# Optimization experiments

Hardware: AMD Instinct MI355X
Metric: run time of the kernel (lower is better)

## Reference

```python
import jax, jax.numpy as jnp
import numpy as np

B, S, D, H, E, K = 4, 2048, 1024, 4096, 4, 2


def setup_inputs() -> dict:
    key = jax.random.key(0)
    ks = jax.random.split(key, 7)
    s1 = 1.0 / np.sqrt(D)  # torch Linear default init bound for fan_in=D
    s2 = 1.0 / np.sqrt(H)
    return {
        "x": jax.random.normal(ks[0], (B, S, D), jnp.float32),
        "w1": jax.random.uniform(ks[1], (E, D, H), jnp.float32, -s1, s1),
        "b1": jax.random.uniform(ks[2], (E, H), jnp.float32, -s1, s1),
        "w2": jax.random.uniform(ks[3], (E, H, D), jnp.float32, -s2, s2),
        "b2": jax.random.uniform(ks[4], (E, D), jnp.float32, -s2, s2),
        "wr": jax.random.uniform(ks[5], (D, E), jnp.float32, -s1, s1),
        "br": jax.random.uniform(ks[6], (E,), jnp.float32, -s1, s1),
    }


def reference(x, w1, b1, w2, b2, wr, br):
    # Faithful to the naive torch SparseMoE (noisy_gating=False):
    #   out += gates[:, i, None] * expert_j(x_flat * mask_ij)  for all i, j
    # Key observation: expert_j applied to a zeroed row gives the constant
    #   c_j = W2_j @ gelu(b1_j) + b2_j  (torch GELU is the exact erf form),
    # so for token t routed (at slot i) to expert e = idx[t, i]:
    #   sum_j expert_j(x_t * mask) = FFN_e(x_t) - c_e + sum_j c_j
    # This reproduces the original math exactly while running each expert's
    # dense FFN over ALL tokens (the naive compute pattern).
    Bx, Sx, Dx = x.shape
    xf = x.reshape(-1, Dx)                                   # [N, D]
    logits = xf @ wr + br                                    # [N, E]
    topk_vals, topk_idx = jax.lax.top_k(logits, K)           # [N, K]
    gates = jax.nn.softmax(topk_vals, axis=-1)               # [N, K]

    # Dense per-expert FFN over all tokens (naive MoE compute)
    h = jax.nn.gelu(jnp.einsum('nd,edh->enh', xf, w1) + b1[:, None, :],
                    approximate=False)                       # [E, N, H]
    y = jnp.einsum('enh,ehd->end', h, w2) + b2[:, None, :]   # [E, N, D]

    # expert_j(0) constants
    c = jnp.einsum('eh,ehd->ed', jax.nn.gelu(b1, approximate=False), w2) + b2  # [E, D]
    c_sum = c.sum(axis=0)                                    # [D]

    yt = jnp.transpose(y, (1, 0, 2))                         # [N, E, D]
    y_sel = jnp.take_along_axis(yt, topk_idx[:, :, None], axis=1)  # [N, K, D]
    c_sel = c[topk_idx]                                      # [N, K, D]

    out = jnp.einsum('nk,nkd->nd', gates, y_sel - c_sel + c_sum[None, None, :])
    return out.reshape(Bx, Sx, Dx)
```

## Files before the change

### kernel.cpp

```cpp
#include <hip/hip_runtime.h>

#define N_TOK 8192
#define DIM   1024
#define HID   4096
#define NEXP  4
#define MAXT  68
#define NSLOT (MAXT*256)

typedef __attribute__((ext_vector_type(8))) _Float16 f16x8;
typedef __attribute__((ext_vector_type(4))) _Float16 f16x4;
typedef __attribute__((ext_vector_type(4))) float    f32x4;

__device__ __forceinline__ float gelu_erf(float v){
    return 0.5f * v * (1.0f + erff(v * 0.70710678118654752440f));
}
__device__ __forceinline__ float gelu_tanh(float v){
    float u = 0.7978845608028654f * v * (1.0f + 0.044715f * v * v);
    float e = __expf(2.0f * u);
    float t = 1.0f - 2.0f / (e + 1.0f);
    return 0.5f * v * (1.0f + t);
}

#define GLDS16(g, s) __builtin_amdgcn_global_load_lds( \
    (const __attribute__((address_space(1))) void*)(g), \
    (__attribute__((address_space(3))) void*)(s), 16, 0, 0)

#define BARRIER() do{ __builtin_amdgcn_s_barrier(); asm volatile("" ::: "memory"); }while(0)
#define VMCNTN(n) asm volatile("s_waitcnt vmcnt(" #n ")" ::: "memory")

__global__ void k_transpose_all(const float* __restrict__ w1, const float* __restrict__ w2,
                                _Float16* __restrict__ w1t, _Float16* __restrict__ w2t){
    __shared__ float tile[32][33];
    int bid = blockIdx.x;
    int z = bid >> 12;
    int i = bid & 4095;
    const float* s; _Float16* d; int R, C, bx, by;
    if (z < 4){ R = DIM; C = HID; bx = i & 127; by = i >> 7;
        s = w1 + (size_t)z * R * C; d = w1t + (size_t)z * R * C; }
    else      { R = HID; C = DIM; bx = i & 31;  by = i >> 5;
        s = w2 + (size_t)(z-4) * R * C; d = w2t + (size_t)(z-4) * R * C; }
    int tx = threadIdx.x & 31, ty = threadIdx.x >> 5;
    int c0 = bx*32, r0 = by*32;
    #pragma unroll
    for (int rr = 0; rr < 32; rr += 8)
        tile[ty+rr][tx] = s[(size_t)(r0+ty+rr)*C + c0+tx];
    __syncthreads();
    #pragma unroll
    for (int rr = 0; rr < 32; rr += 8)
        d[(size_t)(c0+ty+rr)*R + r0+tx] = (_Float16)tile[tx][ty+rr];
}

__global__ void k_gb1(const float* __restrict__ b1, float* __restrict__ gb1, int n){
    int i = blockIdx.x*256 + threadIdx.x;
    if (i < n) gb1[i] = gelu_erf(b1[i]);
}

__global__ void k_cprime_part(const float* __restrict__ w2, const float* __restrict__ gb1,
                              float* __restrict__ part){
    int d = blockIdx.x*256 + threadIdx.x;
    int p = blockIdx.y, e = blockIdx.z;
    float acc = 0.f;
    int h0 = p*(HID/8);
    for (int h = h0; h < h0 + HID/8; ++h)
        acc += gb1[e*HID + h] * w2[((size_t)e*HID + h)*DIM + d];
    part[(size_t)(e*8 + p)*DIM + d] = acc;
}

__global__ void k_cfinal(const float* __restrict__ part, const float* __restrict__ b2,
                         float* __restrict__ cprime, float* __restrict__ csum){
    int d = blockIdx.x*256 + threadIdx.x;
    float cs = 0.f;
    #pragma unroll
    for (int e = 0; e < NEXP; ++e){
        float a = 0.f;
        #pragma unroll
        for (int p = 0; p < 8; ++p) a += part[(size_t)(e*8 + p)*DIM + d];
        cprime[e*DIM + d] = a;
        cs += a + b2[e*DIM + d];
    }
    csum[d] = cs;
}

__global__ void k_route(const float* __restrict__ x, const float* __restrict__ wr,
                        const float* __restrict__ br, _Float16* __restrict__ xb,
                        int* __restrict__ expi, float* __restrict__ gatev){
    int lane = threadIdx.x & 63, w = threadIdx.x >> 6;
    int t = blockIdx.x*4 + w;
    const float4* x4  = (const float4*)(x + (size_t)t*DIM);
    const float4* wr4 = (const float4*)wr;
    f16x4* xb4 = (f16x4*)(xb + (size_t)t*DIM);
    float a0=0.f, a1=0.f, a2=0.f, a3=0.f;
    #pragma unroll
    for (int it = 0; it < 4; ++it){
        int q = it*64 + lane;
        float4 v = x4[q];
        f16x4 h; h[0]=(_Float16)v.x; h[1]=(_Float16)v.y; h[2]=(_Float16)v.z; h[3]=(_Float16)v.w;
        xb4[q] = h;
        int d = q*4;
        float4 w0 = wr4[d], w1v = wr4[d+1], w2v = wr4[d+2], w3v = wr4[d+3];
        a0 += v.x*w0.x + v.y*w1v.x + v.z*w2v.x + v.w*w3v.x;
        a1 += v.x*w0.y + v.y*w1v.y + v.z*w2v.y + v.w*w3v.y;
        a2 += v.x*w0.z + v.y*w1v.z + v.z*w2v.z + v.w*w3v.z;
        a3 += v.x*w0.w + v.y*w1v.w + v.z*w2v.w + v.w*w3v.w;
    }
    #pragma unroll
    for (int off = 32; off; off >>= 1){
        a0 += __shfl_xor(a0, off);
        a1 += __shfl_xor(a1, off);
        a2 += __shfl_xor(a2, off);
        a3 += __shfl_xor(a3, off);
    }
    if (lane == 0){
        float v[4] = {a0+br[0], a1+br[1], a2+br[2], a3+br[3]};
        int e0 = 0; float v0 = v[0];
        #pragma unroll
        for (int e = 1; e < 4; ++e) if (v[e] > v0){ v0 = v[e]; e0 = e; }
        int e1 = -1; float v1 = -1e30f;
        #pragma unroll
        for (int e = 0; e < 4; ++e) if (e != e0 && v[e] > v1){ v1 = v[e]; e1 = e; }
        float ex = expf(v1 - v0);
        float g0 = 1.f/(1.f+ex), g1 = ex/(1.f+ex);
        expi[2*t] = e0; expi[2*t+1] = e1;
        gatev[2*t] = g0; gatev[2*t+1] = g1;
    }
}

__global__ __launch_bounds__(1024)
void k_compact(const int* __restrict__ expi, const float* __restrict__ gatev,
               int* __restrict__ tbase, int* __restrict__ tokl, int* __restrict__ slotof){
    const int e = blockIdx.x;
    const int tid = threadIdx.x, lane = tid & 63, wv = tid >> 6;
    __shared__ int w4[16][4];
    __shared__ int wsum[16];
    int c0=0,c1=0,c2=0,c3=0;
    const int base = tid*16;
    #pragma unroll
    for (int i = 0; i < 16; ++i){
        int v = expi[base+i];
        c0 += (v==0); c1 += (v==1); c2 += (v==2); c3 += (v==3);
    }
    int mysel = (e==0)?c0:(e==1)?c1:(e==2)?c2:c3;
    int r0=c0, r1=c1, r2=c2, r3=c3;
    #pragma unroll
    for (int off = 32; off; off >>= 1){
        r0 += __shfl_xor(r0,off); r1 += __shfl_xor(r1,off);
        r2 += __shfl_xor(r2,off); r3 += __shfl_xor(r3,off);
    }
    if (lane == 0){ w4[wv][0]=r0; w4[wv][1]=r1; w4[wv][2]=r2; w4[wv][3]=r3; }
    int sc = mysel;
    #pragma unroll
    for (int off = 1; off < 64; off <<= 1){
        int tv = __shfl_up(sc, off);
        if (lane >= off) sc += tv;
    }
    if (lane == 63) wsum[wv] = sc;
    __syncthreads();
    int t0=0,t1=0,t2=0,t3=0;
    #pragma unroll
    for (int i = 0; i < 16; ++i){ t0+=w4[i][0]; t1+=w4[i][1]; t2+=w4[i][2]; t3+=w4[i][3]; }
    int n0=(t0+255)>>8, n1=(t1+255)>>8, n2=(t2+255)>>8, n3=(t3+255)>>8;
    int tb1=n0, tb2=n0+n1, tb3=n0+n1+n2, tb4=n0+n1+n2+n3;
    int mybase = ((e==0)?0:(e==1)?tb1:(e==2)?tb2:tb3)*256;
    int cnt_e  = (e==0)?t0:(e==1)?t1:(e==2)?t2:t3;
    int segrows= ((e==0)?n0:(e==1)?n1:(e==2)?n2:n3)*256;
    int wbase = 0;
    for (int i = 0; i < wv; ++i) wbase += wsum[i];
    int myoff = mybase + wbase + sc - mysel;
    #pragma unroll
    for (int i = 0; i < 16; ++i){
        int j = base + i;
        if (expi[j] == e){
            tokl[myoff]  = j >> 1;
            slotof[j] = myoff;
            myoff++;
        }
    }
    for (int i = cnt_e + tid; i < segrows; i += 1024) tokl[mybase + i] = 0;
    if (e == 0 && tid == 0){
        tbase[0]=0; tbase[1]=tb1; tbase[2]=tb2; tbase[3]=tb3; tbase[4]=tb4;
    }
}


#define G_MFMA(RA, RB, NB) \
  _Pragma("unroll") for (int mf_ = 0; mf_ < 4; ++mf_) \
    _Pragma("unroll") for (int nf_ = 0; nf_ < 2; ++nf_) \
      _Pragma("unroll") for (int ks_ = 0; ks_ < 2; ++ks_) \
        acc[mf_][NB+nf_] = __builtin_amdgcn_mfma_f32_16x16x32_f16( \
            RA[mf_][ks_], RB[nf_][ks_], acc[mf_][NB+nf_], 0, 0, 0)

#define G_LDA(CUR) \
  _Pragma("unroll") for (int mf_ = 0; mf_ < 4; ++mf_) \
    _Pragma("unroll") for (int ks_ = 0; ks_ < 2; ++ks_) \
      rA[mf_][ks_] = *(const f16x8*)(smem + (CUR)*32768 + (rbA[mf_] ^ (ks_<<6)))

#define G_LDB(DST, NB, CUR) \
  _Pragma("unroll") for (int nf_ = 0; nf_ < 2; ++nf_) \
    _Pragma("unroll") for (int ks_ = 0; ks_ < 2; ++ks_) \
      DST[nf_][ks_] = *(const f16x8*)(smem + (CUR)*32768 + (rbB[NB+nf_] ^ (ks_<<6)))

#define STG_A(Q, KT) do{ \
    GLDS16(pA[0] + (size_t)(KT)*64, smem + (Q)*32768 + dA0); \
    GLDS16(pA[1] + (size_t)(KT)*64, smem + (Q)*32768 + dA1); \
    GLDS16(pA[2] + (size_t)(KT)*64, smem + (Q)*32768 + dA2); \
    GLDS16(pA[3] + (size_t)(KT)*64, smem + (Q)*32768 + dA3); }while(0)
#define STG_B(Q, KT, G) do{ \
    GLDS16(pB[G][0] + (size_t)(KT)*64, smem + (Q)*32768 + 16384 + dB[G][0]); \
    GLDS16(pB[G][1] + (size_t)(KT)*64, smem + (Q)*32768 + 16384 + dB[G][1]); }while(0)

template<int KDIM, int NDIM, bool G1>
__global__ __launch_bounds__(256, 2)
void k_gemm(const _Float16* __restrict__ Aglob, const _Float16* __restrict__ Bglob,
            const float* __restrict__ b1, const int* __restrict__ tokl,
            const int* __restrict__ tb, _Float16* __restrict__ Cout)
{
    extern __shared__ char smem[];
    const int NT = NDIM/128;
    const int M2 = 2*MAXT;
    const int nwg = M2*NT;
    const int logical = ((int)blockIdx.x & 7)*(nwg>>3) + ((int)blockIdx.x >> 3);
    const int band = logical / (M2*8);
    const int rr_  = logical % (M2*8);
    const int mt = rr_ >> 3, nt = band*8 + (rr_ & 7);
    if (mt >= 2*tb[4]) return;
    const int e = (mt >= 2*tb[1]) + (mt >= 2*tb[2]) + (mt >= 2*tb[3]);
    const int tid = (int)threadIdx.x;
    const int ln = tid & 63, wv = tid >> 6;
    const int wr2 = wv >> 1, wc2 = wv & 1;
    const int lr = ln & 15, lk = ln >> 4;
    const int NK = KDIM/64;

    const _Float16* pA[4];
    const _Float16* pB[2][2];
    int dB[2][2];
    #pragma unroll
    for (int l = 0; l < 4; ++l){
        const int fl = l*256 + wv*64 + ln;
        const int r_ = fl >> 3;
        const int c  = fl & 7;
        const int csw = (c ^ (r_ & 7)) * 8;
        size_t arow;
        if constexpr (G1) arow = (size_t)tokl[mt*128 + r_];
        else              arow = (size_t)(mt*128 + r_);
        pA[l] = Aglob + arow*KDIM + csw;
    }
    const int dA0 = (0*256 + wv*64)*16, dA1 = (1*256 + wv*64)*16;
    const int dA2 = (2*256 + wv*64)*16, dA3 = (3*256 + wv*64)*16;
    #pragma unroll
    for (int g = 0; g < 2; ++g)
      #pragma unroll
      for (int l = 0; l < 2; ++l){
        const int fl = l*256 + wv*64 + ln;
        const int r0 = fl >> 3;
        const int c  = fl & 7;
        const int rowB = (r0 & 31) + ((r0 >> 5) << 6) + g*32;
        const int csw = (c ^ (rowB & 7)) * 8;
        pB[g][l] = Bglob + ((size_t)e*NDIM + nt*128 + rowB)*KDIM + csw;
        const int r00 = (l*256 + wv*64) >> 3;
        dB[g][l] = ((r00 & 31) + ((r00 >> 5) << 6) + g*32) * 128;
      }

    int rbA[4], rbB[4];
    #pragma unroll
    for (int mf = 0; mf < 4; ++mf){
        int row = wr2*64 + mf*16 + lr;
        rbA[mf] = row*128 + ((lk*16) ^ ((row&7)<<4));
    }
    #pragma unroll
    for (int nf = 0; nf < 4; ++nf){
        int row = wc2*64 + nf*16 + lr;
        rbB[nf] = 16384 + row*128 + ((lk*16) ^ ((row&7)<<4));
    }

    f32x4 acc[4][4];
    #pragma unroll
    for (int i = 0; i < 4; ++i)
        #pragma unroll
        for (int j = 0; j < 4; ++j) acc[i][j] = (f32x4){0.f,0.f,0.f,0.f};
    f16x8 rA[4][2], rB0[2][2], rB1[2][2];

    STG_A(0,0); STG_B(0,0,0);
    STG_B(0,0,1);
    STG_A(1,1); STG_B(1,1,0);
    VMCNTN(8);
    BARRIER();

    for (int t = 0; t < NK; ++t){
        const int cur = t & 1;
        G_LDA(cur); G_LDB(rB0, 0, cur);
        if (t+1 < NK){ STG_B(cur^1, t+1, 1); VMCNTN(8); } else { VMCNTN(0); }
        BARRIER();
        __builtin_amdgcn_s_setprio(1); G_MFMA(rA, rB0, 0); __builtin_amdgcn_s_setprio(0);
        BARRIER();
        G_LDB(rB1, 2, cur);
        if (t+2 < NK){ STG_A(cur, t+2); STG_B(cur, t+2, 0); VMCNTN(8); }
        else if (t+1 < NK){ VMCNTN(2); }
        else { VMCNTN(0); }
        BARRIER();
        __builtin_amdgcn_s_setprio(1); G_MFMA(rA, rB1, 2); __builtin_amdgcn_s_setprio(0);
        BARRIER();
    }

    if constexpr (G1){
        float bv[4];
        #pragma unroll
        for (int nf = 0; nf < 4; ++nf)
            bv[nf] = b1[e*NDIM + nt*128 + wc2*64 + nf*16 + lr];
        #pragma unroll
        for (int mf = 0; mf < 4; ++mf){
            int row = mt*128 + wr2*64 + mf*16 + lk*4;
            #pragma unroll
            for (int nf = 0; nf < 4; ++nf){
                int col = nt*128 + wc2*64 + nf*16 + lr;
                #pragma unroll
                for (int r = 0; r < 4; ++r)
                    Cout[(size_t)(row+r)*NDIM + col] = (_Float16)gelu_tanh(acc[mf][nf][r] + bv[nf]);
            }
        }
    } else {
        #pragma unroll
        for (int mf = 0; mf < 4; ++mf){
            int row = mt*128 + wr2*64 + mf*16 + lk*4;
            #pragma unroll
            for (int nf = 0; nf < 4; ++nf){
                int col = nt*128 + wc2*64 + nf*16 + lr;
                #pragma unroll
                for (int r = 0; r < 4; ++r)
                    Cout[(size_t)(row+r)*NDIM + col] = (_Float16)acc[mf][nf][r];
            }
        }
    }
}

__global__ void k_final(const int* __restrict__ expi, const float* __restrict__ gatev,
                        const int* __restrict__ slotof, const _Float16* __restrict__ ybuf,
                        const float* __restrict__ cprime, const float* __restrict__ csum,
                        float* __restrict__ out){
    int i = blockIdx.x*256 + threadIdx.x;
    int t = i >> 8;
    int dq = i & 255;
    int e0 = expi[2*t], e1 = expi[2*t+1];
    float g0 = gatev[2*t], g1 = gatev[2*t+1];
    int s0 = slotof[2*t], s1 = slotof[2*t+1];
    const float4* cp = (const float4*)cprime;
    float4 cs = ((const float4*)csum)[dq];
    float4 c0 = cp[e0*256 + dq], c1 = cp[e1*256 + dq];
    f16x4 y0 = ((const f16x4*)ybuf)[(size_t)s0*256 + dq];
    f16x4 y1 = ((const f16x4*)ybuf)[(size_t)s1*256 + dq];
    float4 r;
    r.x = cs.x + g0*((float)y0[0] - c0.x) + g1*((float)y1[0] - c1.x);
    r.y = cs.y + g0*((float)y0[1] - c0.y) + g1*((float)y1[1] - c1.y);
    r.z = cs.z + g0*((float)y0[2] - c0.z) + g1*((float)y1[2] - c1.z);
    r.w = cs.w + g0*((float)y0[3] - c0.w) + g1*((float)y1[3] - c1.w);
    ((float4*)out)[i] = r;
}

extern "C" void kernel_launch(void* const* d_in, const int* in_sizes, int n_in,
                              void* d_out, int out_size, void* d_ws, size_t ws_size,
                              hipStream_t stream){
    const float* x  = (const float*)d_in[0];
    const float* w1 = (const float*)d_in[1];
    const float* b1 = (const float*)d_in[2];
    const float* w2 = (const float*)d_in[3];
    const float* b2 = (const float*)d_in[4];
    const float* wr = (const float*)d_in[5];
    const float* br = (const float*)d_in[6];
    float* out = (float*)d_out;

    char* ws = (char*)d_ws;
    size_t o = 0;
    auto take = [&](size_t bytes)->char*{
        char* p = ws + o;
        o = (o + bytes + 255) & ~(size_t)255;
        return p;
    };
    _Float16* xb    = (_Float16*)take((size_t)N_TOK*DIM*2);
    _Float16* w1t   = (_Float16*)take((size_t)NEXP*HID*DIM*2);
    _Float16* w2t   = (_Float16*)take((size_t)NEXP*HID*DIM*2);
    _Float16* hbuf  = (_Float16*)take((size_t)NSLOT*HID*2);
    _Float16* ybuf  = (_Float16*)take((size_t)NSLOT*DIM*2);
    float*    gb1   = (float*)take((size_t)NEXP*HID*4);
    float*    part  = (float*)take((size_t)NEXP*8*DIM*4);
    float*    cprime= (float*)take((size_t)NEXP*DIM*4);
    float*    csum  = (float*)take((size_t)DIM*4);
    int*      tbase = (int*)take(64);
    int*      expi  = (int*)take((size_t)N_TOK*2*4);
    float*    gatev = (float*)take((size_t)N_TOK*2*4);
    int*      slotof= (int*)take((size_t)N_TOK*2*4);
    int*      tokl  = (int*)take((size_t)NSLOT*4);
    (void)ws_size; (void)in_sizes; (void)n_in; (void)out_size;

    hipFuncSetAttribute(reinterpret_cast<const void*>(&k_gemm<DIM, HID, true>),
                        hipFuncAttributeMaxDynamicSharedMemorySize, 65536);
    hipFuncSetAttribute(reinterpret_cast<const void*>(&k_gemm<HID, DIM, false>),
                        hipFuncAttributeMaxDynamicSharedMemorySize, 65536);

    hipLaunchKernelGGL(k_transpose_all, dim3(32768), dim3(256), 0, stream, w1, w2, w1t, w2t);
    hipLaunchKernelGGL(k_gb1, dim3(NEXP*HID/256), dim3(256), 0, stream, b1, gb1, NEXP*HID);
    hipLaunchKernelGGL(k_cprime_part, dim3(DIM/256, 8, NEXP), dim3(256), 0, stream, w2, gb1, part);
    hipLaunchKernelGGL(k_cfinal, dim3(DIM/256), dim3(256), 0, stream, part, b2, cprime, csum);
    hipLaunchKernelGGL(k_route, dim3(N_TOK/4), dim3(256), 0, stream, x, wr, br, xb, expi, gatev);
    hipLaunchKernelGGL(k_compact, dim3(NEXP), dim3(1024), 0, stream, expi, gatev, tbase, tokl, slotof);
    hipLaunchKernelGGL((k_gemm<DIM, HID, true>), dim3(2*MAXT*(HID/128)), dim3(256), 65536, stream,
                       xb, w1t, b1, tokl, tbase, hbuf);
    hipLaunchKernelGGL((k_gemm<HID, DIM, false>), dim3(2*MAXT*(DIM/128)), dim3(256), 65536, stream,
                       hbuf, w2t, b1, tokl, tbase, ybuf);
    hipLaunchKernelGGL(k_final, dim3(N_TOK*DIM/4/256), dim3(256), 0, stream,
                       expi, gatev, slotof, ybuf, cprime, csum, out);
}
```

Baseline: 441.4 us.

## Halve GEMM K-tile to 32 with paired-row swizzle for higher occupancy

The expert GEMM K-step shrinks from 64 to 32, which halves shared memory per block to 32 KB and the A/B fragment registers. Launch bounds rise to 4 blocks per CU. A new LDS layout packs two rows per 128-byte line with an XOR swizzle to keep bank conflicts low. The aim is more resident waves to hide memory latency, at the cost of twice as many loop iterations and barriers per tile and less work between synchronisations.

```diff
diff --git a/kernel.cpp b/kernel.cpp
--- a/kernel.cpp
+++ b/kernel.cpp
@@ -185,31 +185,25 @@
 #define G_MFMA(RA, RB, NB) \
   _Pragma("unroll") for (int mf_ = 0; mf_ < 4; ++mf_) \
     _Pragma("unroll") for (int nf_ = 0; nf_ < 2; ++nf_) \
-      _Pragma("unroll") for (int ks_ = 0; ks_ < 2; ++ks_) \
         acc[mf_][NB+nf_] = __builtin_amdgcn_mfma_f32_16x16x32_f16( \
-            RA[mf_][ks_], RB[nf_][ks_], acc[mf_][NB+nf_], 0, 0, 0)
+            RA[mf_], RB[nf_], acc[mf_][NB+nf_], 0, 0, 0)
 
 #define G_LDA(CUR) \
   _Pragma("unroll") for (int mf_ = 0; mf_ < 4; ++mf_) \
-    _Pragma("unroll") for (int ks_ = 0; ks_ < 2; ++ks_) \
-      rA[mf_][ks_] = *(const f16x8*)(smem + (CUR)*32768 + (rbA[mf_] ^ (ks_<<6)))
+      rA[mf_] = *(const f16x8*)(smem + (CUR)*16384 + rbA[mf_])
 
 #define G_LDB(DST, NB, CUR) \
   _Pragma("unroll") for (int nf_ = 0; nf_ < 2; ++nf_) \
-    _Pragma("unroll") for (int ks_ = 0; ks_ < 2; ++ks_) \
-      DST[nf_][ks_] = *(const f16x8*)(smem + (CUR)*32768 + (rbB[NB+nf_] ^ (ks_<<6)))
+      DST[nf_] = *(const f16x8*)(smem + (CUR)*16384 + rbB[NB+nf_])
 
 #define STG_A(Q, KT) do{ \
-    GLDS16(pA[0] + (size_t)(KT)*64, smem + (Q)*32768 + dA0); \
-    GLDS16(pA[1] + (size_t)(KT)*64, smem + (Q)*32768 + dA1); \
-    GLDS16(pA[2] + (size_t)(KT)*64, smem + (Q)*32768 + dA2); \
-    GLDS16(pA[3] + (size_t)(KT)*64, smem + (Q)*32768 + dA3); }while(0)
-#define STG_B(Q, KT, G) do{ \
-    GLDS16(pB[G][0] + (size_t)(KT)*64, smem + (Q)*32768 + 16384 + dB[G][0]); \
-    GLDS16(pB[G][1] + (size_t)(KT)*64, smem + (Q)*32768 + 16384 + dB[G][1]); }while(0)
+    GLDS16(pA[0] + (size_t)(KT)*32, smem + (Q)*16384 + dA0); \
+    GLDS16(pA[1] + (size_t)(KT)*32, smem + (Q)*16384 + dA1); }while(0)
+#define STG_B0(Q, KT) GLDS16(pB0 + (size_t)(KT)*32, smem + (Q)*16384 + 8192 + dB0)
+#define STG_B1(Q, KT) GLDS16(pB1 + (size_t)(KT)*32, smem + (Q)*16384 + 8192 + dB1)
 
 template<int KDIM, int NDIM, bool G1>
-__global__ __launch_bounds__(256, 2)
+__global__ __launch_bounds__(256, 4)
 void k_gemm(const _Float16* __restrict__ Aglob, const _Float16* __restrict__ Bglob,
             const float* __restrict__ b1, const int* __restrict__ tokl,
             const int* __restrict__ tb, _Float16* __restrict__ Cout)
@@ -228,48 +222,54 @@
     const int ln = tid & 63, wv = tid >> 6;
     const int wr2 = wv >> 1, wc2 = wv & 1;
     const int lr = ln & 15, lk = ln >> 4;
-    const int NK = KDIM/64;
-
-    const _Float16* pA[4];
-    const _Float16* pB[2][2];
-    int dB[2][2];
-    #pragma unroll
-    for (int l = 0; l < 4; ++l){
-        const int fl = l*256 + wv*64 + ln;
-        const int r_ = fl >> 3;
-        const int c  = fl & 7;
-        const int csw = (c ^ (r_ & 7)) * 8;
+    const int NK = KDIM/32;
+
+    const _Float16* pA[2];
+    #pragma unroll
+    for (int l = 0; l < 2; ++l){
+        const int p  = (wv*2 + l)*8 + (ln >> 3);
+        const int sp = (ln & 7) ^ (p & 7);
+        const int row = 2*p + (sp >> 2);
+        const int kc  = sp & 3;
         size_t arow;
-        if constexpr (G1) arow = (size_t)tokl[mt*128 + r_];
-        else              arow = (size_t)(mt*128 + r_);
-        pA[l] = Aglob + arow*KDIM + csw;
-    }
-    const int dA0 = (0*256 + wv*64)*16, dA1 = (1*256 + wv*64)*16;
-    const int dA2 = (2*256 + wv*64)*16, dA3 = (3*256 + wv*64)*16;
-    #pragma unroll
-    for (int g = 0; g < 2; ++g)
-      #pragma unroll
-      for (int l = 0; l < 2; ++l){
-        const int fl = l*256 + wv*64 + ln;
-        const int r0 = fl >> 3;
-        const int c  = fl & 7;
-        const int rowB = (r0 & 31) + ((r0 >> 5) << 6) + g*32;
-        const int csw = (c ^ (rowB & 7)) * 8;
-        pB[g][l] = Bglob + ((size_t)e*NDIM + nt*128 + rowB)*KDIM + csw;
-        const int r00 = (l*256 + wv*64) >> 3;
-        dB[g][l] = ((r00 & 31) + ((r00 >> 5) << 6) + g*32) * 128;
-      }
+        if constexpr (G1) arow = (size_t)tokl[mt*128 + row];
+        else              arow = (size_t)(mt*128 + row);
+        pA[l] = Aglob + arow*KDIM + kc*8;
+    }
+    const int dA0 = (wv*2+0)*1024 + 0;
+    const int dA1 = (wv*2+1)*1024 + 0;
+    const int pb0s = (wv & 1)*8 + (wv >> 1)*32;
+    const int pb1s = pb0s + 16;
+    const _Float16* pB0; const _Float16* pB1;
+    {
+        const int p  = pb0s + (ln >> 3);
+        const int sp = (ln & 7) ^ (p & 7);
+        const int row = 2*p + (sp >> 2);
+        const int kc  = sp & 3;
+        pB0 = Bglob + ((size_t)e*NDIM + nt*128 + row)*KDIM + kc*8;
+    }
+    {
+        const int p  = pb1s + (ln >> 3);
+        const int sp = (ln & 7) ^ (p & 7);
+        const int row = 2*p + (sp >> 2);
+        const int kc  = sp & 3;
+        pB1 = Bglob + ((size_t)e*NDIM + nt*128 + row)*KDIM + kc*8;
+    }
+    const int dB0 = pb0s*128;
+    const int dB1 = pb1s*128;
 
     int rbA[4], rbB[4];
     #pragma unroll
     for (int mf = 0; mf < 4; ++mf){
         int row = wr2*64 + mf*16 + lr;
-        rbA[mf] = row*128 + ((lk*16) ^ ((row&7)<<4));
+        int p = row >> 1, sp = (row & 1)*4 + lk;
+        rbA[mf] = p*128 + (sp ^ (p & 7))*16;
     }
     #pragma unroll
     for (int nf = 0; nf < 4; ++nf){
         int row = wc2*64 + nf*16 + lr;
-        rbB[nf] = 16384 + row*128 + ((lk*16) ^ ((row&7)<<4));
+        int p = row >> 1, sp = (row & 1)*4 + lk;
+        rbB[nf] = 8192 + p*128 + (sp ^ (p & 7))*16;
     }
 
     f32x4 acc[4][4];
@@ -277,24 +277,24 @@
     for (int i = 0; i < 4; ++i)
         #pragma unroll
         for (int j = 0; j < 4; ++j) acc[i][j] = (f32x4){0.f,0.f,0.f,0.f};
-    f16x8 rA[4][2], rB0[2][2], rB1[2][2];
-
-    STG_A(0,0); STG_B(0,0,0);
-    STG_B(0,0,1);
-    STG_A(1,1); STG_B(1,1,0);
-    VMCNTN(8);
+    f16x8 rA[4], rB0[2], rB1[2];
+
+    STG_A(0,0); STG_B0(0,0);
+    STG_B1(0,0);
+    STG_A(1,1); STG_B0(1,1);
+    VMCNTN(4);
     BARRIER();
 
     for (int t = 0; t < NK; ++t){
         const int cur = t & 1;
         G_LDA(cur); G_LDB(rB0, 0, cur);
-        if (t+1 < NK){ STG_B(cur^1, t+1, 1); VMCNTN(8); } else { VMCNTN(0); }
+        if (t+1 < NK){ STG_B1(cur^1, t+1); VMCNTN(4); } else { VMCNTN(0); }
         BARRIER();
         __builtin_amdgcn_s_setprio(1); G_MFMA(rA, rB0, 0); __builtin_amdgcn_s_setprio(0);
         BARRIER();
         G_LDB(rB1, 2, cur);
-        if (t+2 < NK){ STG_A(cur, t+2); STG_B(cur, t+2, 0); VMCNTN(8); }
-        else if (t+1 < NK){ VMCNTN(2); }
+        if (t+2 < NK){ STG_A(cur, t+2); STG_B0(cur, t+2); VMCNTN(4); }
+        else if (t+1 < NK){ VMCNTN(1); }
         else { VMCNTN(0); }
         BARRIER();
         __builtin_amdgcn_s_setprio(1); G_MFMA(rA, rB1, 2); __builtin_amdgcn_s_setprio(0);
@@ -391,9 +391,9 @@
     (void)ws_size; (void)in_sizes; (void)n_in; (void)out_size;
 
     hipFuncSetAttribute(reinterpret_cast<const void*>(&k_gemm<DIM, HID, true>),
-                        hipFuncAttributeMaxDynamicSharedMemorySize, 65536);
+                        hipFuncAttributeMaxDynamicSharedMemorySize, 32768);
     hipFuncSetAttribute(reinterpret_cast<const void*>(&k_gemm<HID, DIM, false>),
-                        hipFuncAttributeMaxDynamicSharedMemorySize, 65536);
+                        hipFuncAttributeMaxDynamicSharedMemorySize, 32768);
 
     hipLaunchKernelGGL(k_transpose_all, dim3(32768), dim3(256), 0, stream, w1, w2, w1t, w2t);
     hipLaunchKernelGGL(k_gb1, dim3(NEXP*HID/256), dim3(256), 0, stream, b1, gb1, NEXP*HID);
@@ -401,9 +401,9 @@
     hipLaunchKernelGGL(k_cfinal, dim3(DIM/256), dim3(256), 0, stream, part, b2, cprime, csum);
     hipLaunchKernelGGL(k_route, dim3(N_TOK/4), dim3(256), 0, stream, x, wr, br, xb, expi, gatev);
     hipLaunchKernelGGL(k_compact, dim3(NEXP), dim3(1024), 0, stream, expi, gatev, tbase, tokl, slotof);
-    hipLaunchKernelGGL((k_gemm<DIM, HID, true>), dim3(2*MAXT*(HID/128)), dim3(256), 65536, stream,
+    hipLaunchKernelGGL((k_gemm<DIM, HID, true>), dim3(2*MAXT*(HID/128)), dim3(256), 32768, stream,
                        xb, w1t, b1, tokl, tbase, hbuf);
-    hipLaunchKernelGGL((k_gemm<HID, DIM, false>), dim3(2*MAXT*(DIM/128)), dim3(256), 65536, stream,
+    hipLaunchKernelGGL((k_gemm<HID, DIM, false>), dim3(2*MAXT*(DIM/128)), dim3(256), 32768, stream,
                        hbuf, w2t, b1, tokl, tbase, ybuf);
     hipLaunchKernelGGL(k_final, dim3(N_TOK*DIM/4/256), dim3(256), 0, stream,
                        expi, gatev, slotof, ybuf, cprime, csum, out);
```

After: 495.9 us. +12.4%, slower.
